# Kernel optimization log

Hardware: AMD Instinct MI355X
Metric: run time of the kernel (lower is better)

Reference implementation:

```python
import jax, jax.numpy as jnp
import numpy as np

B, D, N, MSRC, H = 4, 256, 2048, 2048, 4
DIM = D // H  # per-head dim = 64
EPS = 1e-3


def _conv1x1(W, b, z):
    # 1x1 Conv1d == per-position linear: W [out,in], z [B,in,N]
    return jnp.einsum('oc,bcn->bon', W, z) + b[None, :, None]


def setup_inputs() -> dict:
    key = jax.random.key(0)
    ks = jax.random.split(key, 20)
    s = 0.05
    x = jax.random.normal(ks[0], (B, D, N), dtype=jnp.float32)
    source = jax.random.normal(ks[1], (B, D, MSRC), dtype=jnp.float32)
    mask = (jax.random.uniform(ks[2], (B, N, MSRC)) > 0.3).astype(jnp.float32)
    Wq = jax.random.normal(ks[3], (D, D), jnp.float32) * s
    bq = jax.random.normal(ks[4], (D,), jnp.float32) * s
    Wk = jax.random.normal(ks[5], (D, D), jnp.float32) * s
    bk = jax.random.normal(ks[6], (D,), jnp.float32) * s
    Wv = jax.random.normal(ks[7], (D, D), jnp.float32) * s
    bv = jax.random.normal(ks[8], (D,), jnp.float32) * s
    Wm = jax.random.normal(ks[9], (D, D), jnp.float32) * s
    bm = jax.random.normal(ks[10], (D,), jnp.float32) * s
    W1 = jax.random.normal(ks[11], (2 * D, 2 * D), jnp.float32) * s
    b1 = jax.random.normal(ks[12], (2 * D,), jnp.float32) * s
    gamma = jnp.ones((2 * D,), jnp.float32)
    beta = jnp.zeros((2 * D,), jnp.float32)
    rmean = jax.random.normal(ks[13], (2 * D,), jnp.float32) * 0.1
    rvar = jax.random.uniform(ks[14], (2 * D,), jnp.float32) + 0.5
    W2 = jax.random.normal(ks[15], (D, 2 * D), jnp.float32) * s
    b2 = jnp.zeros((D,), jnp.float32)  # nn.init.constant_(mlp[-1].bias, 0.0)
    return dict(x=x, source=source, mask=mask, Wq=Wq, bq=bq, Wk=Wk, bk=bk,
                Wv=Wv, bv=bv, Wm=Wm, bm=bm, W1=W1, b1=b1, gamma=gamma,
                beta=beta, rmean=rmean, rvar=rvar, W2=W2, b2=b2)


def reference(x, source, mask, Wq, bq, Wk, bk, Wv, bv, Wm, bm,
              W1, b1, gamma, beta, rmean, rvar, W2, b2):
    b = x.shape[0]
    # channel dim split as (dim, heads) per torch .view(B, dim, H, -1)
    q = _conv1x1(Wq, bq, x).reshape(b, DIM, H, -1)        # [B,d,H,N]
    k = _conv1x1(Wk, bk, source).reshape(b, DIM, H, -1)   # [B,d,H,M]
    v = _conv1x1(Wv, bv, source).reshape(b, DIM, H, -1)   # [B,d,H,M]
    scores = jnp.einsum('bdhn,bdhm->bhnm', q, k) / (DIM ** 0.5)
    neg = -jnp.finfo(scores.dtype).max
    scores = jnp.where(mask[:, None, :, :] > 0, scores, neg)
    prob = jax.nn.softmax(scores, axis=-1)                # [B,H,N,M]
    msg = jnp.einsum('bhnm,bdhm->bdhn', prob, v).reshape(b, D, -1)
    message = _conv1x1(Wm, bm, msg)                       # [B,D,N]
    y = jnp.concatenate([x, message], axis=1)             # [B,2D,N]
    h = _conv1x1(W1, b1, y)
    # BatchNorm1d (eval mode, eps=1e-3)
    h = (h - rmean[None, :, None]) * jax.lax.rsqrt(rvar + EPS)[None, :, None]
    h = h * gamma[None, :, None] + beta[None, :, None]
    h = jax.nn.relu(h)
    return _conv1x1(W2, b2, h)                            # [B,D,N]
```

## Files before the change

### kernel.cpp

```cpp
#include <hip/hip_runtime.h>

constexpr int Bb = 4;
constexpr int Dd = 256;
constexpr int Nn = 2048;
constexpr int Mm = 2048;
constexpr int Hh = 4;
constexpr int D2 = 512;
constexpr int NT = Bb * Nn;

#define FMAXV 3.402823466e38f

typedef _Float16 half8 __attribute__((ext_vector_type(8)));
typedef _Float16 half4v __attribute__((ext_vector_type(4)));
typedef float f32x4 __attribute__((ext_vector_type(4)));

typedef const __attribute__((address_space(1))) void* gas_p;
typedef __attribute__((address_space(3))) void* las_p;

__device__ __forceinline__ void gload16(const void* g, void* l) {
    __builtin_amdgcn_global_load_lds((gas_p)g, (las_p)l, 16, 0, 0);
}

__global__ __launch_bounds__(256)
void prep_weights_kernel(const float* __restrict__ Wq, const float* __restrict__ bq,
                         const float* __restrict__ Wk, const float* __restrict__ bk,
                         const float* __restrict__ Wv, const float* __restrict__ bv,
                         const float* __restrict__ Wm,
                         const float* __restrict__ W1, const float* __restrict__ b1,
                         const float* __restrict__ gamma, const float* __restrict__ beta,
                         const float* __restrict__ rmean, const float* __restrict__ rvar,
                         const float* __restrict__ W2, const float* __restrict__ mask,
                         _Float16* __restrict__ Wqp, float* __restrict__ bqp,
                         _Float16* __restrict__ Wkvp, float* __restrict__ bkvp,
                         _Float16* __restrict__ Wmp,
                         _Float16* __restrict__ W1p, float* __restrict__ b1f,
                         _Float16* __restrict__ W2p,
                         unsigned long long* __restrict__ bmask) {
    const int r = blockIdx.x, t = threadIdx.x;
    if (r < 256) {
        const int h = r >> 6, d = r & 63, so = d * Hh + h;
        Wqp[r * 256 + t] = (_Float16)Wq[so * 256 + t];
        if (t == 0) bqp[r] = bq[so];
    } else if (r < 768) {
        const int rr = r - 256, part = rr >> 8, o = rr & 255;
        const int h = o >> 6, d = o & 63, so = d * Hh + h;
        const float* Ws = part ? Wv : Wk;
        const float* bs = part ? bv : bk;
        Wkvp[rr * 256 + t] = (_Float16)Ws[so * 256 + t];
        if (t == 0) bkvp[rr] = bs[so];
    } else if (r < 1024) {
        const int o = r - 768;
        const int h = t >> 6, d = t & 63, sk = d * Hh + h;
        Wmp[o * 256 + t] = (_Float16)Wm[o * 256 + sk];
    } else if (r < 1536) {
        const int o = r - 1024;
        const float s = gamma[o] * rsqrtf(rvar[o] + 1e-3f);
        W1p[o * 512 + t]       = (_Float16)(W1[o * 512 + t] * s);
        W1p[o * 512 + t + 256] = (_Float16)(W1[o * 512 + t + 256] * s);
        if (t == 0) b1f[o] = (b1[o] - rmean[o]) * s + beta[o];
    } else if (r < 1792) {
        const int o = r - 1536;
        W2p[o * 512 + t]       = (_Float16)W2[o * 512 + t];
        W2p[o * 512 + t + 256] = (_Float16)W2[o * 512 + t + 256];
    } else {
        const int id = r - 1792;
        const int w = t >> 6, lane = t & 63;
        const int row = id * 4 + w;
        const float* mrow = mask + (size_t)row * Mm;
        unsigned long long* brow = bmask + (size_t)row * (Mm / 64);
        #pragma unroll 4
        for (int word = 0; word < Mm / 64; ++word) {
            const float v = mrow[word * 64 + lane];
            const unsigned long long bits = __ballot(v > 0.f);
            if (lane == 0) brow[word] = bits;
        }
    }
}

__global__ __launch_bounds__(256)
void prep_x_kernel(const float* __restrict__ x, const float* __restrict__ source,
                   _Float16* __restrict__ Yp, _Float16* __restrict__ Sp) {
    __shared__ _Float16 Ts[64][72];
    const int z = blockIdx.z, b = z >> 1, which = z & 1;
    const float* src = which ? source : x;
    _Float16* dst = which ? Sp : Yp;
    const int stride = which ? 256 : 512;
    const int c0 = blockIdx.y * 64, n0 = blockIdx.x * 64;
    const int t = threadIdx.x;
    const int cl = t >> 2, np = (t & 3) * 16;
    const float* sp = src + ((size_t)b * Dd + c0 + cl) * Nn + n0 + np;
    #pragma unroll
    for (int i = 0; i < 4; ++i) {
        float4 v = *(const float4*)(sp + i * 4);
        Ts[np + i * 4 + 0][cl] = (_Float16)v.x;
        Ts[np + i * 4 + 1][cl] = (_Float16)v.y;
        Ts[np + i * 4 + 2][cl] = (_Float16)v.z;
        Ts[np + i * 4 + 3][cl] = (_Float16)v.w;
    }
    __syncthreads();
    const int nl = t >> 2, cp = (t & 3) * 16;
    half8 a0 = *(const half8*)&Ts[nl][cp];
    half8 a1 = *(const half8*)&Ts[nl][cp + 8];
    _Float16* dp = dst + ((size_t)b * Nn + n0 + nl) * stride + c0 + cp;
    *(half8*)dp = a0;
    *(half8*)(dp + 8) = a1;
}

__global__ __launch_bounds__(256)
void gemm4w_kernel(const _Float16* __restrict__ A, const _Float16* __restrict__ A2,
                   const _Float16* __restrict__ W, const float* __restrict__ bias,
                   _Float16* __restrict__ dst0, _Float16* __restrict__ dst1,
                   _Float16* __restrict__ dst2, float* __restrict__ dstF,
                   int K, int sA, int sOut, int modeSel, int relu) {
    __shared__ __align__(16) _Float16 As[2][128][64];
    __shared__ __align__(16) _Float16 Bs[2][128][64];
    __shared__ __align__(16) _Float16 Es[4][16][72];

    const int t = threadIdx.x;
    const int w = t >> 6, lane = t & 63, quad = lane >> 4, l16 = lane & 15;
    const int wr = w >> 1, wc = w & 1;
    const int n0 = blockIdx.x * 128;
    const int og0 = blockIdx.y * 128;

    int mode = 0, oloc0 = og0;
    const _Float16* Ab = A;
    int sAl = sA;
    _Float16* d0 = dst0;
    if (modeSel == 3) {
        const int part = blockIdx.y >> 1;
        if (part == 1)      { Ab = A2; sAl = 256; d0 = dst1; oloc0 = og0 - 256; }
        else if (part == 2) { Ab = A2; sAl = 256; mode = 1; oloc0 = og0 - 512; }
    } else if (modeSel == 2) {
        mode = 2;
    }

    const int srow = t >> 3, sslot = t & 7;
    const int schunk = sslot ^ (srow & 7);

    f32x4 acc[4][4] = {};

    const int nk = K / 64;
    int buf = 0;

    {
        #pragma unroll
        for (int c = 0; c < 4; ++c) {
            const int row = c * 32 + srow;
            gload16(Ab + (size_t)(n0 + row) * sAl + schunk * 8,
                    (_Float16*)As + c * 2048 + t * 8);
            gload16(W + (size_t)(og0 + row) * K + schunk * 8,
                    (_Float16*)Bs + c * 2048 + t * 8);
        }
        __asm__ volatile("s_waitcnt vmcnt(0)" ::: "memory");
        __syncthreads();
    }

    #pragma unroll 1
    for (int kt = 0; kt < nk; ++kt) {
        if (kt + 1 < nk) {
            const int k0 = (kt + 1) * 64, nb = buf ^ 1;
            #pragma unroll
            for (int c = 0; c < 4; ++c) {
                const int row = c * 32 + srow;
                gload16(Ab + (size_t)(n0 + row) * sAl + k0 + schunk * 8,
                        (_Float16*)As + nb * 8192 + c * 2048 + t * 8);
                gload16(W + (size_t)(og0 + row) * K + k0 + schunk * 8,
                        (_Float16*)Bs + nb * 8192 + c * 2048 + t * 8);
            }
        }
        #pragma unroll
        for (int ks = 0; ks < 2; ++ks) {
            const int csw = ((ks * 4 + quad) ^ (l16 & 7)) * 8;
            half8 af[4], bf[4];
            #pragma unroll
            for (int i = 0; i < 4; ++i)
                af[i] = *(const half8*)&As[buf][wr * 64 + i * 16 + l16][csw];
            #pragma unroll
            for (int j = 0; j < 4; ++j)
                bf[j] = *(const half8*)&Bs[buf][wc * 64 + j * 16 + l16][csw];
            #pragma unroll
            for (int i = 0; i < 4; ++i)
                #pragma unroll
                for (int j = 0; j < 4; ++j)
                    acc[i][j] = __builtin_amdgcn_mfma_f32_16x16x32_f16(af[i], bf[j], acc[i][j], 0, 0, 0);
        }
        if (kt + 1 < nk) {
            __asm__ volatile("s_waitcnt vmcnt(0)" ::: "memory");
            __syncthreads();
            buf ^= 1;
        }
    }

    float bcol[4];
    #pragma unroll
    for (int j = 0; j < 4; ++j) bcol[j] = bias[og0 + wc * 64 + j * 16 + l16];

    if (mode == 0) {
        #pragma unroll
        for (int i = 0; i < 4; ++i) {
            #pragma unroll
            for (int j = 0; j < 4; ++j)
                #pragma unroll
                for (int reg = 0; reg < 4; ++reg) {
                    float v = acc[i][j][reg] + bcol[j];
                    if (relu) v = fmaxf(v, 0.f);
                    Es[w][quad * 4 + reg][j * 16 + l16] = (_Float16)v;
                }
            __asm__ volatile("s_waitcnt lgkmcnt(0)" ::: "memory");
            const int row = lane & 15, oseg = (lane >> 4) * 16;
            half8 e0 = *(const half8*)&Es[w][row][oseg];
            half8 e1 = *(const half8*)&Es[w][row][oseg + 8];
            _Float16* dp = d0 + (size_t)(n0 + wr * 64 + i * 16 + row) * sOut
                         + oloc0 + wc * 64 + oseg;
            *(half8*)dp = e0;
            *(half8*)(dp + 8) = e1;
            __asm__ volatile("s_waitcnt lgkmcnt(0)" ::: "memory");
        }
    } else if (mode == 1) {
        #pragma unroll
        for (int i = 0; i < 4; ++i) {
            const int ng = n0 + wr * 64 + i * 16 + quad * 4;
            const int bidx = ng >> 11, m0 = ng & 2047;
            #pragma unroll
            for (int j = 0; j < 4; ++j) {
                const int o = oloc0 + wc * 64 + j * 16 + l16;
                half4v pv;
                #pragma unroll
                for (int reg = 0; reg < 4; ++reg) pv[reg] = (_Float16)(acc[i][j][reg] + bcol[j]);
                *(half4v*)(dst2 + ((size_t)bidx * 256 + o) * (size_t)Mm + m0) = pv;
            }
        }
    } else {
        #pragma unroll
        for (int i = 0; i < 4; ++i) {
            const int ng = n0 + wr * 64 + i * 16 + quad * 4;
            const int bidx = ng >> 11, m0 = ng & 2047;
            #pragma unroll
            for (int j = 0; j < 4; ++j) {
                const int o = og0 + wc * 64 + j * 16 + l16;
                f32x4 v;
                #pragma unroll
                for (int reg = 0; reg < 4; ++reg) v[reg] = acc[i][j][reg] + bcol[j];
                *(f32x4*)(dstF + ((size_t)bidx * 256 + o) * (size_t)Nn + m0) = v;
            }
        }
    }
}

__global__ __launch_bounds__(256)
void attn_mfma_kernel(const _Float16* __restrict__ Qp, const _Float16* __restrict__ Kp,
                      const _Float16* __restrict__ Vt,
                      const unsigned int* __restrict__ bmask,
                      _Float16* __restrict__ msgp) {
    __shared__ __align__(16) _Float16 Ks[2][64][72];
    __shared__ __align__(16) _Float16 Vs[2][64][72];
    __shared__ __align__(16) _Float16 Ps[4][16][72];

    const int b = blockIdx.z, h = blockIdx.y, n0 = blockIdx.x * 64;
    const int t = threadIdx.x;
    const int w = t >> 6, lane = t & 63, quad = lane >> 4, l16 = lane & 15;

    const _Float16* qp = Qp + ((size_t)b * Nn + n0 + w * 16 + l16) * 256 + h * 64 + quad * 8;
    const half8 qa0 = *(const half8*)(qp);
    const half8 qa1 = *(const half8*)(qp + 32);

    const _Float16* Kstg = Kp + (size_t)b * Nn * 256 + h * 64;
    const _Float16* Vstg = Vt + ((size_t)b * 256 + h * 64) * (size_t)Mm;
    const int sr = t >> 2, sc = (t & 3) * 16;

    const unsigned int* bmBase = bmask + ((size_t)b * Nn + n0 + w * 16 + quad * 4) * (Mm / 32);

    float lo[4] = {0.f, 0.f, 0.f, 0.f};
    f32x4 O[4] = {};

    half8 sk0, sk1, sv0, sv1;
    auto stage_load = [&](int m0) {
        const _Float16* ks = Kstg + (size_t)(m0 + sr) * 256 + sc;
        sk0 = *(const half8*)(ks);
        sk1 = *(const half8*)(ks + 8);
        const _Float16* vs = Vstg + (size_t)sr * Mm + m0 + sc;
        sv0 = *(const half8*)(vs);
        sv1 = *(const half8*)(vs + 8);
    };
    auto stage_write = [&](int buf) {
        *(half8*)&Ks[buf][sr][sc]     = sk0;
        *(half8*)&Ks[buf][sr][sc + 8] = sk1;
        *(half8*)&Vs[buf][sr][sc]     = sv0;
        *(half8*)&Vs[buf][sr][sc + 8] = sv1;
    };

    stage_load(0);
    stage_write(0);
    __syncthreads();

    #pragma unroll 1
    for (int it = 0; it < Mm / 64; ++it) {
        const int m0 = it * 64, cur = it & 1;
        if (it < Mm / 64 - 1) stage_load(m0 + 64);

        uint2 bmv[4];
        #pragma unroll
        for (int reg = 0; reg < 4; ++reg)
            bmv[reg] = *(const uint2*)(bmBase + (size_t)reg * (Mm / 32) + (m0 >> 5));

        f32x4 S[4];
        #pragma unroll
        for (int mt = 0; mt < 4; ++mt) {
            half8 k0 = *(const half8*)&Ks[cur][mt * 16 + l16][quad * 8];
            half8 k1 = *(const half8*)&Ks[cur][mt * 16 + l16][32 + quad * 8];
            f32x4 z = {0.f, 0.f, 0.f, 0.f};
            z = __builtin_amdgcn_mfma_f32_16x16x32_f16(qa0, k0, z, 0, 0, 0);
            z = __builtin_amdgcn_mfma_f32_16x16x32_f16(qa1, k1, z, 0, 0, 0);
            S[mt] = z;
        }

        float p[4][4];
        #pragma unroll
        for (int reg = 0; reg < 4; ++reg) {
            const unsigned losh = bmv[reg].x >> l16;
            const unsigned hish = bmv[reg].y >> l16;
            p[0][reg] = (losh & 1u)         ? __expf(S[0][reg] * 0.125f) : 0.f;
            p[1][reg] = ((losh >> 16) & 1u) ? __expf(S[1][reg] * 0.125f) : 0.f;
            p[2][reg] = (hish & 1u)         ? __expf(S[2][reg] * 0.125f) : 0.f;
            p[3][reg] = ((hish >> 16) & 1u) ? __expf(S[3][reg] * 0.125f) : 0.f;
        }
        #pragma unroll
        for (int reg = 0; reg < 4; ++reg)
            lo[reg] += (p[0][reg] + p[1][reg]) + (p[2][reg] + p[3][reg]);

        #pragma unroll
        for (int mt = 0; mt < 4; ++mt)
            #pragma unroll
            for (int reg = 0; reg < 4; ++reg)
                Ps[w][quad * 4 + reg][mt * 16 + l16] = (_Float16)p[mt][reg];
        __asm__ volatile("s_waitcnt lgkmcnt(0)" ::: "memory");
        half8 pa0 = *(const half8*)&Ps[w][l16][quad * 8];
        half8 pa1 = *(const half8*)&Ps[w][l16][32 + quad * 8];

        #pragma unroll
        for (int dt = 0; dt < 4; ++dt) {
            half8 v0 = *(const half8*)&Vs[cur][dt * 16 + l16][quad * 8];
            half8 v1 = *(const half8*)&Vs[cur][dt * 16 + l16][32 + quad * 8];
            O[dt] = __builtin_amdgcn_mfma_f32_16x16x32_f16(pa0, v0, O[dt], 0, 0, 0);
            O[dt] = __builtin_amdgcn_mfma_f32_16x16x32_f16(pa1, v1, O[dt], 0, 0, 0);
        }

        if (it < Mm / 64 - 1) stage_write(cur ^ 1);
        __syncthreads();
    }

    #pragma unroll
    for (int reg = 0; reg < 4; ++reg) {
        float s = lo[reg];
        s += __shfl_xor(s, 1);
        s += __shfl_xor(s, 2);
        s += __shfl_xor(s, 4);
        s += __shfl_xor(s, 8);
        lo[reg] = 1.0f / s;
    }

    _Float16* op = msgp + ((size_t)b * Nn + n0 + w * 16 + quad * 4) * 256 + h * 64 + l16;
    #pragma unroll
    for (int reg = 0; reg < 4; ++reg)
        #pragma unroll
        for (int dt = 0; dt < 4; ++dt)
            op[(size_t)reg * 256 + dt * 16] = (_Float16)(O[dt][reg] * lo[reg]);
}

extern "C" void kernel_launch(void* const* d_in, const int* in_sizes, int n_in,
                              void* d_out, int out_size, void* d_ws, size_t ws_size,
                              hipStream_t stream) {
    const float* x      = (const float*)d_in[0];
    const float* source = (const float*)d_in[1];
    const float* mask   = (const float*)d_in[2];
    const float* Wq = (const float*)d_in[3];
    const float* bq = (const float*)d_in[4];
    const float* Wk = (const float*)d_in[5];
    const float* bk = (const float*)d_in[6];
    const float* Wv = (const float*)d_in[7];
    const float* bv = (const float*)d_in[8];
    const float* Wm = (const float*)d_in[9];
    const float* bm = (const float*)d_in[10];
    const float* W1 = (const float*)d_in[11];
    const float* b1 = (const float*)d_in[12];
    const float* gamma = (const float*)d_in[13];
    const float* beta  = (const float*)d_in[14];
    const float* rmean = (const float*)d_in[15];
    const float* rvar  = (const float*)d_in[16];
    const float* W2 = (const float*)d_in[17];
    const float* b2 = (const float*)d_in[18];
    float* outp = (float*)d_out;

    char* wsb = (char*)d_ws;
    _Float16* Yp   = (_Float16*)wsb;
    _Float16* Sp   = (_Float16*)(wsb + (8u << 20));
    _Float16* Qp   = (_Float16*)(wsb + (12u << 20));
    _Float16* Kp   = (_Float16*)(wsb + (16u << 20));
    _Float16* Vt   = (_Float16*)(wsb + (20u << 20));
    _Float16* msgp = (_Float16*)(wsb + (24u << 20));
    _Float16* Hp   = (_Float16*)(wsb + (28u << 20));
    unsigned long long* bmask = (unsigned long long*)(wsb + (28u << 20));
    char* wp = wsb + (36u << 20);
    _Float16* Wqp  = (_Float16*)wp;            wp += 256 * 256 * 2;
    _Float16* Wkvp = (_Float16*)wp;            wp += 512 * 256 * 2;
    _Float16* Wmp  = (_Float16*)wp;            wp += 256 * 256 * 2;
    _Float16* W1p  = (_Float16*)wp;            wp += 512 * 512 * 2;
    _Float16* W2p  = (_Float16*)wp;            wp += 256 * 512 * 2;
    float* bqp  = (float*)wp;                  wp += 256 * 4;
    float* bkvp = (float*)wp;                  wp += 512 * 4;
    float* b1f  = (float*)wp;                  wp += 512 * 4;

    prep_weights_kernel<<<3840, 256, 0, stream>>>(
        Wq, bq, Wk, bk, Wv, bv, Wm, W1, b1, gamma, beta, rmean, rvar, W2, mask,
        Wqp, bqp, Wkvp, bkvp, Wmp, W1p, b1f, W2p, bmask);

    dim3 gPrep(Nn / 64, Dd / 64, Bb * 2);
    prep_x_kernel<<<gPrep, 256, 0, stream>>>(x, source, Yp, Sp);

    gemm4w_kernel<<<dim3(NT / 128, 6), 256, 0, stream>>>(
        Yp, Sp, Wqp, bqp, Qp, Kp, Vt, nullptr, 256, 512, 256, 3, 0);

    dim3 gAttn(Nn / 64, Hh, Bb);
    attn_mfma_kernel<<<gAttn, 256, 0, stream>>>(Qp, Kp, Vt,
                                                (const unsigned int*)bmask, msgp);

    gemm4w_kernel<<<dim3(NT / 128, 2), 256, 0, stream>>>(
        msgp, nullptr, Wmp, bm, Yp + 256, nullptr, nullptr, nullptr, 256, 256, 512, 0, 0);
    gemm4w_kernel<<<dim3(NT / 128, 4), 256, 0, stream>>>(
        Yp, nullptr, W1p, b1f, Hp, nullptr, nullptr, nullptr, 512, 512, 512, 0, 1);
    gemm4w_kernel<<<dim3(NT / 128, 2), 256, 0, stream>>>(
        Hp, nullptr, W2p, b2, nullptr, nullptr, nullptr, outp, 512, 512, 0, 2, 0);
}
```

Baseline: 248.8 us.

## Split attention over key halves, shrink GEMM tiles, fuse prep kernels

Attention is split into two halves along the key dimension with an XCD-aware block mapping. Each half writes unnormalized partial outputs and row sums, and a new combine kernel merges them. This is meant to double the attention grid for better occupancy. The 1/sqrt(d) scale is folded into the Q projection epilogue, and the attention tile drops double-buffered LDS in favour of extra syncs. GEMM output tiles shrink from 128x128 to 128x64 to double the block count, and the x/source transpose prep is merged into the weight prep kernel to save a launch. Risks are the extra combine pass, extra partial-result traffic, and the extra barriers in attention.

```diff
diff --git a/kernel.cpp b/kernel.cpp
--- a/kernel.cpp
+++ b/kernel.cpp
@@ -22,20 +22,22 @@
 }
 
 __global__ __launch_bounds__(256)
-void prep_weights_kernel(const float* __restrict__ Wq, const float* __restrict__ bq,
-                         const float* __restrict__ Wk, const float* __restrict__ bk,
-                         const float* __restrict__ Wv, const float* __restrict__ bv,
-                         const float* __restrict__ Wm,
-                         const float* __restrict__ W1, const float* __restrict__ b1,
-                         const float* __restrict__ gamma, const float* __restrict__ beta,
-                         const float* __restrict__ rmean, const float* __restrict__ rvar,
-                         const float* __restrict__ W2, const float* __restrict__ mask,
-                         _Float16* __restrict__ Wqp, float* __restrict__ bqp,
-                         _Float16* __restrict__ Wkvp, float* __restrict__ bkvp,
-                         _Float16* __restrict__ Wmp,
-                         _Float16* __restrict__ W1p, float* __restrict__ b1f,
-                         _Float16* __restrict__ W2p,
-                         unsigned long long* __restrict__ bmask) {
+void prep_all_kernel(const float* __restrict__ Wq, const float* __restrict__ bq,
+                     const float* __restrict__ Wk, const float* __restrict__ bk,
+                     const float* __restrict__ Wv, const float* __restrict__ bv,
+                     const float* __restrict__ Wm,
+                     const float* __restrict__ W1, const float* __restrict__ b1,
+                     const float* __restrict__ gamma, const float* __restrict__ beta,
+                     const float* __restrict__ rmean, const float* __restrict__ rvar,
+                     const float* __restrict__ W2, const float* __restrict__ mask,
+                     const float* __restrict__ x, const float* __restrict__ source,
+                     _Float16* __restrict__ Wqp, float* __restrict__ bqp,
+                     _Float16* __restrict__ Wkvp, float* __restrict__ bkvp,
+                     _Float16* __restrict__ Wmp,
+                     _Float16* __restrict__ W1p, float* __restrict__ b1f,
+                     _Float16* __restrict__ W2p,
+                     unsigned long long* __restrict__ bmask,
+                     _Float16* __restrict__ Yp, _Float16* __restrict__ Sp) {
     const int r = blockIdx.x, t = threadIdx.x;
     if (r < 256) {
         const int h = r >> 6, d = r & 63, so = d * Hh + h;
@@ -62,7 +64,7 @@
         const int o = r - 1536;
         W2p[o * 512 + t]       = (_Float16)W2[o * 512 + t];
         W2p[o * 512 + t + 256] = (_Float16)W2[o * 512 + t + 256];
-    } else {
+    } else if (r < 3840) {
         const int id = r - 1792;
         const int w = t >> 6, lane = t & 63;
         const int row = id * 4 + w;
@@ -74,36 +76,32 @@
             const unsigned long long bits = __ballot(v > 0.f);
             if (lane == 0) brow[word] = bits;
         }
-    }
-}
-
-__global__ __launch_bounds__(256)
-void prep_x_kernel(const float* __restrict__ x, const float* __restrict__ source,
-                   _Float16* __restrict__ Yp, _Float16* __restrict__ Sp) {
-    __shared__ _Float16 Ts[64][72];
-    const int z = blockIdx.z, b = z >> 1, which = z & 1;
-    const float* src = which ? source : x;
-    _Float16* dst = which ? Sp : Yp;
-    const int stride = which ? 256 : 512;
-    const int c0 = blockIdx.y * 64, n0 = blockIdx.x * 64;
-    const int t = threadIdx.x;
-    const int cl = t >> 2, np = (t & 3) * 16;
-    const float* sp = src + ((size_t)b * Dd + c0 + cl) * Nn + n0 + np;
-    #pragma unroll
-    for (int i = 0; i < 4; ++i) {
-        float4 v = *(const float4*)(sp + i * 4);
-        Ts[np + i * 4 + 0][cl] = (_Float16)v.x;
-        Ts[np + i * 4 + 1][cl] = (_Float16)v.y;
-        Ts[np + i * 4 + 2][cl] = (_Float16)v.z;
-        Ts[np + i * 4 + 3][cl] = (_Float16)v.w;
-    }
-    __syncthreads();
-    const int nl = t >> 2, cp = (t & 3) * 16;
-    half8 a0 = *(const half8*)&Ts[nl][cp];
-    half8 a1 = *(const half8*)&Ts[nl][cp + 8];
-    _Float16* dp = dst + ((size_t)b * Nn + n0 + nl) * stride + c0 + cp;
-    *(half8*)dp = a0;
-    *(half8*)(dp + 8) = a1;
+    } else {
+        __shared__ _Float16 Ts[64][72];
+        const int px = r - 3840;
+        const int n0 = (px & 31) * 64, c0 = ((px >> 5) & 3) * 64;
+        const int z = px >> 7, b = z >> 1, which = z & 1;
+        const float* src = which ? source : x;
+        _Float16* dst = which ? Sp : Yp;
+        const int stride = which ? 256 : 512;
+        const int cl = t >> 2, np = (t & 3) * 16;
+        const float* sp = src + ((size_t)b * Dd + c0 + cl) * Nn + n0 + np;
+        #pragma unroll
+        for (int i = 0; i < 4; ++i) {
+            float4 v = *(const float4*)(sp + i * 4);
+            Ts[np + i * 4 + 0][cl] = (_Float16)v.x;
+            Ts[np + i * 4 + 1][cl] = (_Float16)v.y;
+            Ts[np + i * 4 + 2][cl] = (_Float16)v.z;
+            Ts[np + i * 4 + 3][cl] = (_Float16)v.w;
+        }
+        __syncthreads();
+        const int nl = t >> 2, cp = (t & 3) * 16;
+        half8 a0 = *(const half8*)&Ts[nl][cp];
+        half8 a1 = *(const half8*)&Ts[nl][cp + 8];
+        _Float16* dp = dst + ((size_t)b * Nn + n0 + nl) * stride + c0 + cp;
+        *(half8*)dp = a0;
+        *(half8*)(dp + 8) = a1;
+    }
 }
 
 __global__ __launch_bounds__(256)
@@ -111,25 +109,25 @@
                    const _Float16* __restrict__ W, const float* __restrict__ bias,
                    _Float16* __restrict__ dst0, _Float16* __restrict__ dst1,
                    _Float16* __restrict__ dst2, float* __restrict__ dstF,
-                   int K, int sA, int sOut, int modeSel, int relu) {
-    __shared__ __align__(16) _Float16 As[2][128][64];
-    __shared__ __align__(16) _Float16 Bs[2][128][64];
+                   int K, int sA, int sOut, int modeSel, int relu, float oscale) {
+    __shared__ __align__(16) _Float16 As[2 * 128 * 64];
+    __shared__ __align__(16) _Float16 Bs[2 * 64 * 64];
     __shared__ __align__(16) _Float16 Es[4][16][72];
 
     const int t = threadIdx.x;
     const int w = t >> 6, lane = t & 63, quad = lane >> 4, l16 = lane & 15;
-    const int wr = w >> 1, wc = w & 1;
     const int n0 = blockIdx.x * 128;
-    const int og0 = blockIdx.y * 128;
+    const int og0 = blockIdx.y * 64;
 
     int mode = 0, oloc0 = og0;
     const _Float16* Ab = A;
     int sAl = sA;
     _Float16* d0 = dst0;
+    float osc = oscale;
     if (modeSel == 3) {
-        const int part = blockIdx.y >> 1;
-        if (part == 1)      { Ab = A2; sAl = 256; d0 = dst1; oloc0 = og0 - 256; }
-        else if (part == 2) { Ab = A2; sAl = 256; mode = 1; oloc0 = og0 - 512; }
+        const int part = blockIdx.y >> 2;
+        if (part == 1)      { Ab = A2; sAl = 256; d0 = dst1; oloc0 = og0 - 256; osc = 1.0f; }
+        else if (part == 2) { Ab = A2; sAl = 256; mode = 1; oloc0 = og0 - 512; osc = 1.0f; }
     } else if (modeSel == 2) {
         mode = 2;
     }
@@ -137,20 +135,19 @@
     const int srow = t >> 3, sslot = t & 7;
     const int schunk = sslot ^ (srow & 7);
 
-    f32x4 acc[4][4] = {};
-
+    f32x4 acc[2][4] = {};
     const int nk = K / 64;
     int buf = 0;
 
     {
         #pragma unroll
-        for (int c = 0; c < 4; ++c) {
-            const int row = c * 32 + srow;
-            gload16(Ab + (size_t)(n0 + row) * sAl + schunk * 8,
-                    (_Float16*)As + c * 2048 + t * 8);
-            gload16(W + (size_t)(og0 + row) * K + schunk * 8,
-                    (_Float16*)Bs + c * 2048 + t * 8);
-        }
+        for (int c = 0; c < 4; ++c)
+            gload16(Ab + (size_t)(n0 + c * 32 + srow) * sAl + schunk * 8,
+                    As + c * 2048 + t * 8);
+        #pragma unroll
+        for (int c = 0; c < 2; ++c)
+            gload16(W + (size_t)(og0 + c * 32 + srow) * K + schunk * 8,
+                    Bs + c * 2048 + t * 8);
         __asm__ volatile("s_waitcnt vmcnt(0)" ::: "memory");
         __syncthreads();
     }
@@ -160,26 +157,26 @@
         if (kt + 1 < nk) {
             const int k0 = (kt + 1) * 64, nb = buf ^ 1;
             #pragma unroll
-            for (int c = 0; c < 4; ++c) {
-                const int row = c * 32 + srow;
-                gload16(Ab + (size_t)(n0 + row) * sAl + k0 + schunk * 8,
-                        (_Float16*)As + nb * 8192 + c * 2048 + t * 8);
-                gload16(W + (size_t)(og0 + row) * K + k0 + schunk * 8,
-                        (_Float16*)Bs + nb * 8192 + c * 2048 + t * 8);
-            }
+            for (int c = 0; c < 4; ++c)
+                gload16(Ab + (size_t)(n0 + c * 32 + srow) * sAl + k0 + schunk * 8,
+                        As + nb * 8192 + c * 2048 + t * 8);
+            #pragma unroll
+            for (int c = 0; c < 2; ++c)
+                gload16(W + (size_t)(og0 + c * 32 + srow) * K + k0 + schunk * 8,
+                        Bs + nb * 4096 + c * 2048 + t * 8);
         }
         #pragma unroll
         for (int ks = 0; ks < 2; ++ks) {
             const int csw = ((ks * 4 + quad) ^ (l16 & 7)) * 8;
-            half8 af[4], bf[4];
-            #pragma unroll
-            for (int i = 0; i < 4; ++i)
-                af[i] = *(const half8*)&As[buf][wr * 64 + i * 16 + l16][csw];
+            half8 af[2], bf[4];
+            #pragma unroll
+            for (int i = 0; i < 2; ++i)
+                af[i] = *(const half8*)&As[buf * 8192 + (w * 32 + i * 16 + l16) * 64 + csw];
             #pragma unroll
             for (int j = 0; j < 4; ++j)
-                bf[j] = *(const half8*)&Bs[buf][wc * 64 + j * 16 + l16][csw];
-            #pragma unroll
-            for (int i = 0; i < 4; ++i)
+                bf[j] = *(const half8*)&Bs[buf * 4096 + (j * 16 + l16) * 64 + csw];
+            #pragma unroll
+            for (int i = 0; i < 2; ++i)
                 #pragma unroll
                 for (int j = 0; j < 4; ++j)
                     acc[i][j] = __builtin_amdgcn_mfma_f32_16x16x32_f16(af[i], bf[j], acc[i][j], 0, 0, 0);
@@ -193,16 +190,16 @@
 
     float bcol[4];
     #pragma unroll
-    for (int j = 0; j < 4; ++j) bcol[j] = bias[og0 + wc * 64 + j * 16 + l16];
+    for (int j = 0; j < 4; ++j) bcol[j] = bias[og0 + j * 16 + l16];
 
     if (mode == 0) {
         #pragma unroll
-        for (int i = 0; i < 4; ++i) {
+        for (int i = 0; i < 2; ++i) {
             #pragma unroll
             for (int j = 0; j < 4; ++j)
                 #pragma unroll
                 for (int reg = 0; reg < 4; ++reg) {
-                    float v = acc[i][j][reg] + bcol[j];
+                    float v = (acc[i][j][reg] + bcol[j]) * osc;
                     if (relu) v = fmaxf(v, 0.f);
                     Es[w][quad * 4 + reg][j * 16 + l16] = (_Float16)v;
                 }
@@ -210,20 +207,19 @@
             const int row = lane & 15, oseg = (lane >> 4) * 16;
             half8 e0 = *(const half8*)&Es[w][row][oseg];
             half8 e1 = *(const half8*)&Es[w][row][oseg + 8];
-            _Float16* dp = d0 + (size_t)(n0 + wr * 64 + i * 16 + row) * sOut
-                         + oloc0 + wc * 64 + oseg;
+            _Float16* dp = d0 + (size_t)(n0 + w * 32 + i * 16 + row) * sOut + oloc0 + oseg;
             *(half8*)dp = e0;
             *(half8*)(dp + 8) = e1;
             __asm__ volatile("s_waitcnt lgkmcnt(0)" ::: "memory");
         }
     } else if (mode == 1) {
         #pragma unroll
-        for (int i = 0; i < 4; ++i) {
-            const int ng = n0 + wr * 64 + i * 16 + quad * 4;
+        for (int i = 0; i < 2; ++i) {
+            const int ng = n0 + w * 32 + i * 16 + quad * 4;
             const int bidx = ng >> 11, m0 = ng & 2047;
             #pragma unroll
             for (int j = 0; j < 4; ++j) {
-                const int o = oloc0 + wc * 64 + j * 16 + l16;
+                const int o = oloc0 + j * 16 + l16;
                 half4v pv;
                 #pragma unroll
                 for (int reg = 0; reg < 4; ++reg) pv[reg] = (_Float16)(acc[i][j][reg] + bcol[j]);
@@ -232,12 +228,12 @@
         }
     } else {
         #pragma unroll
-        for (int i = 0; i < 4; ++i) {
-            const int ng = n0 + wr * 64 + i * 16 + quad * 4;
+        for (int i = 0; i < 2; ++i) {
+            const int ng = n0 + w * 32 + i * 16 + quad * 4;
             const int bidx = ng >> 11, m0 = ng & 2047;
             #pragma unroll
             for (int j = 0; j < 4; ++j) {
-                const int o = og0 + wc * 64 + j * 16 + l16;
+                const int o = og0 + j * 16 + l16;
                 f32x4 v;
                 #pragma unroll
                 for (int reg = 0; reg < 4; ++reg) v[reg] = acc[i][j][reg] + bcol[j];
@@ -251,12 +247,20 @@
 void attn_mfma_kernel(const _Float16* __restrict__ Qp, const _Float16* __restrict__ Kp,
                       const _Float16* __restrict__ Vt,
                       const unsigned int* __restrict__ bmask,
-                      _Float16* __restrict__ msgp) {
-    __shared__ __align__(16) _Float16 Ks[2][64][72];
-    __shared__ __align__(16) _Float16 Vs[2][64][72];
+                      _Float16* __restrict__ Oa, _Float16* __restrict__ Ob,
+                      float* __restrict__ La, float* __restrict__ Lb) {
+    __shared__ __align__(16) _Float16 Ks[64][72];
+    __shared__ __align__(16) _Float16 Vs[64][72];
     __shared__ __align__(16) _Float16 Ps[4][16][72];
 
-    const int b = blockIdx.z, h = blockIdx.y, n0 = blockIdx.x * 64;
+    const int id = blockIdx.x;
+    const int xcd = id & 7, loc = id >> 3;
+    const int bh = xcd * 2 + (loc >> 6);
+    const int sub = loc & 63;
+    const int mhalf = sub & 1;
+    const int n0 = (sub >> 1) * 64;
+    const int b = bh >> 2, h = bh & 3;
+
     const int t = threadIdx.x;
     const int w = t >> 6, lane = t & 63, quad = lane >> 4, l16 = lane & 15;
 
@@ -269,6 +273,10 @@
     const int sr = t >> 2, sc = (t & 3) * 16;
 
     const unsigned int* bmBase = bmask + ((size_t)b * Nn + n0 + w * 16 + quad * 4) * (Mm / 32);
+
+    _Float16* Od = mhalf ? Ob : Oa;
+    float* Ld = mhalf ? Lb : La;
+    const int mbeg = mhalf * (Mm / 2);
 
     float lo[4] = {0.f, 0.f, 0.f, 0.f};
     f32x4 O[4] = {};
@@ -282,21 +290,21 @@
         sv0 = *(const half8*)(vs);
         sv1 = *(const half8*)(vs + 8);
     };
-    auto stage_write = [&](int buf) {
-        *(half8*)&Ks[buf][sr][sc]     = sk0;
-        *(half8*)&Ks[buf][sr][sc + 8] = sk1;
-        *(half8*)&Vs[buf][sr][sc]     = sv0;
-        *(half8*)&Vs[buf][sr][sc + 8] = sv1;
+    auto stage_write = [&]() {
+        *(half8*)&Ks[sr][sc]     = sk0;
+        *(half8*)&Ks[sr][sc + 8] = sk1;
+        *(half8*)&Vs[sr][sc]     = sv0;
+        *(half8*)&Vs[sr][sc + 8] = sv1;
     };
 
-    stage_load(0);
-    stage_write(0);
+    stage_load(mbeg);
+    stage_write();
     __syncthreads();
 
     #pragma unroll 1
-    for (int it = 0; it < Mm / 64; ++it) {
-        const int m0 = it * 64, cur = it & 1;
-        if (it < Mm / 64 - 1) stage_load(m0 + 64);
+    for (int it = 0; it < (Mm / 2) / 64; ++it) {
+        const int m0 = mbeg + it * 64;
+        if (it < (Mm / 2) / 64 - 1) stage_load(m0 + 64);
 
         uint2 bmv[4];
         #pragma unroll
@@ -306,8 +314,8 @@
         f32x4 S[4];
         #pragma unroll
         for (int mt = 0; mt < 4; ++mt) {
-            half8 k0 = *(const half8*)&Ks[cur][mt * 16 + l16][quad * 8];
-            half8 k1 = *(const half8*)&Ks[cur][mt * 16 + l16][32 + quad * 8];
+            half8 k0 = *(const half8*)&Ks[mt * 16 + l16][quad * 8];
+            half8 k1 = *(const half8*)&Ks[mt * 16 + l16][32 + quad * 8];
             f32x4 z = {0.f, 0.f, 0.f, 0.f};
             z = __builtin_amdgcn_mfma_f32_16x16x32_f16(qa0, k0, z, 0, 0, 0);
             z = __builtin_amdgcn_mfma_f32_16x16x32_f16(qa1, k1, z, 0, 0, 0);
@@ -319,10 +327,10 @@
         for (int reg = 0; reg < 4; ++reg) {
             const unsigned losh = bmv[reg].x >> l16;
             const unsigned hish = bmv[reg].y >> l16;
-            p[0][reg] = (losh & 1u)         ? __expf(S[0][reg] * 0.125f) : 0.f;
-            p[1][reg] = ((losh >> 16) & 1u) ? __expf(S[1][reg] * 0.125f) : 0.f;
-            p[2][reg] = (hish & 1u)         ? __expf(S[2][reg] * 0.125f) : 0.f;
-            p[3][reg] = ((hish >> 16) & 1u) ? __expf(S[3][reg] * 0.125f) : 0.f;
+            p[0][reg] = (losh & 1u)         ? __expf(S[0][reg]) : 0.f;
+            p[1][reg] = ((losh >> 16) & 1u) ? __expf(S[1][reg]) : 0.f;
+            p[2][reg] = (hish & 1u)         ? __expf(S[2][reg]) : 0.f;
+            p[3][reg] = ((hish >> 16) & 1u) ? __expf(S[3][reg]) : 0.f;
         }
         #pragma unroll
         for (int reg = 0; reg < 4; ++reg)
@@ -339,14 +347,17 @@
 
         #pragma unroll
         for (int dt = 0; dt < 4; ++dt) {
-            half8 v0 = *(const half8*)&Vs[cur][dt * 16 + l16][quad * 8];
-            half8 v1 = *(const half8*)&Vs[cur][dt * 16 + l16][32 + quad * 8];
+            half8 v0 = *(const half8*)&Vs[dt * 16 + l16][quad * 8];
+            half8 v1 = *(const half8*)&Vs[dt * 16 + l16][32 + quad * 8];
             O[dt] = __builtin_amdgcn_mfma_f32_16x16x32_f16(pa0, v0, O[dt], 0, 0, 0);
             O[dt] = __builtin_amdgcn_mfma_f32_16x16x32_f16(pa1, v1, O[dt], 0, 0, 0);
         }
 
-        if (it < Mm / 64 - 1) stage_write(cur ^ 1);
-        __syncthreads();
+        if (it < (Mm / 2) / 64 - 1) {
+            __syncthreads();
+            stage_write();
+            __syncthreads();
+        }
     }
 
     #pragma unroll
@@ -356,15 +367,38 @@
         s += __shfl_xor(s, 2);
         s += __shfl_xor(s, 4);
         s += __shfl_xor(s, 8);
-        lo[reg] = 1.0f / s;
-    }
-
-    _Float16* op = msgp + ((size_t)b * Nn + n0 + w * 16 + quad * 4) * 256 + h * 64 + l16;
+        lo[reg] = s;
+    }
+
+    _Float16* op = Od + ((size_t)b * Nn + n0 + w * 16 + quad * 4) * 256 + h * 64 + l16;
     #pragma unroll
     for (int reg = 0; reg < 4; ++reg)
         #pragma unroll
         for (int dt = 0; dt < 4; ++dt)
-            op[(size_t)reg * 256 + dt * 16] = (_Float16)(O[dt][reg] * lo[reg]);
+            op[(size_t)reg * 256 + dt * 16] = (_Float16)(O[dt][reg] * 0.0625f);
+    if (l16 == 0) {
+        #pragma unroll
+        for (int reg = 0; reg < 4; ++reg)
+            Ld[((size_t)b * Nn + n0 + w * 16 + quad * 4 + reg) * 4 + h] = lo[reg] * 0.0625f;
+    }
+}
+
+__global__ __launch_bounds__(256)
+void combine_kernel(const _Float16* __restrict__ Oa, const _Float16* __restrict__ Ob,
+                    const float* __restrict__ La, const float* __restrict__ Lb,
+                    _Float16* __restrict__ out) {
+    const int gid = blockIdx.x * 256 + threadIdx.x;
+    const int row = gid >> 5, chunk = gid & 31;
+    const int h = chunk >> 3;
+    const float L = La[row * 4 + h] + Lb[row * 4 + h];
+    const float inv = 1.0f / L;
+    half8 a = *(const half8*)(Oa + (size_t)row * 256 + chunk * 8);
+    half8 c = *(const half8*)(Ob + (size_t)row * 256 + chunk * 8);
+    half8 o;
+    #pragma unroll
+    for (int k = 0; k < 8; ++k)
+        o[k] = (_Float16)(((float)a[k] + (float)c[k]) * inv);
+    *(half8*)(out + (size_t)row * 256 + chunk * 8) = o;
 }
 
 extern "C" void kernel_launch(void* const* d_in, const int* in_sizes, int n_in,
@@ -400,6 +434,9 @@
     _Float16* msgp = (_Float16*)(wsb + (24u << 20));
     _Float16* Hp   = (_Float16*)(wsb + (28u << 20));
     unsigned long long* bmask = (unsigned long long*)(wsb + (28u << 20));
+    _Float16* Ob = (_Float16*)(wsb + (30u << 20));
+    float* La = (float*)(wsb + (34u << 20));
+    float* Lb = (float*)(wsb + (34u << 20) + (128u << 10));
     char* wp = wsb + (36u << 20);
     _Float16* Wqp  = (_Float16*)wp;            wp += 256 * 256 * 2;
     _Float16* Wkvp = (_Float16*)wp;            wp += 512 * 256 * 2;
@@ -410,24 +447,23 @@
     float* bkvp = (float*)wp;                  wp += 512 * 4;
     float* b1f  = (float*)wp;                  wp += 512 * 4;
 
-    prep_weights_kernel<<<3840, 256, 0, stream>>>(
+    prep_all_kernel<<<4864, 256, 0, stream>>>(
         Wq, bq, Wk, bk, Wv, bv, Wm, W1, b1, gamma, beta, rmean, rvar, W2, mask,
-        Wqp, bqp, Wkvp, bkvp, Wmp, W1p, b1f, W2p, bmask);
-
-    dim3 gPrep(Nn / 64, Dd / 64, Bb * 2);
-    prep_x_kernel<<<gPrep, 256, 0, stream>>>(x, source, Yp, Sp);
-
-    gemm4w_kernel<<<dim3(NT / 128, 6), 256, 0, stream>>>(
-        Yp, Sp, Wqp, bqp, Qp, Kp, Vt, nullptr, 256, 512, 256, 3, 0);
-
-    dim3 gAttn(Nn / 64, Hh, Bb);
-    attn_mfma_kernel<<<gAttn, 256, 0, stream>>>(Qp, Kp, Vt,
-                                                (const unsigned int*)bmask, msgp);
-
-    gemm4w_kernel<<<dim3(NT / 128, 2), 256, 0, stream>>>(
-        msgp, nullptr, Wmp, bm, Yp + 256, nullptr, nullptr, nullptr, 256, 256, 512, 0, 0);
+        x, source, Wqp, bqp, Wkvp, bkvp, Wmp, W1p, b1f, W2p, bmask, Yp, Sp);
+
+    gemm4w_kernel<<<dim3(NT / 128, 12), 256, 0, stream>>>(
+        Yp, Sp, Wqp, bqp, Qp, Kp, Vt, nullptr, 256, 512, 256, 3, 0, 0.125f);
+
+    attn_mfma_kernel<<<1024, 256, 0, stream>>>(Qp, Kp, Vt,
+                                               (const unsigned int*)bmask,
+                                               msgp, Ob, La, Lb);
+
+    combine_kernel<<<1024, 256, 0, stream>>>(msgp, Ob, La, Lb, Sp);
+
     gemm4w_kernel<<<dim3(NT / 128, 4), 256, 0, stream>>>(
-        Yp, nullptr, W1p, b1f, Hp, nullptr, nullptr, nullptr, 512, 512, 512, 0, 1);
-    gemm4w_kernel<<<dim3(NT / 128, 2), 256, 0, stream>>>(
-        Hp, nullptr, W2p, b2, nullptr, nullptr, nullptr, outp, 512, 512, 0, 2, 0);
-}
+        Sp, nullptr, Wmp, bm, Yp + 256, nullptr, nullptr, nullptr, 256, 256, 512, 0, 0, 1.0f);
+    gemm4w_kernel<<<dim3(NT / 128, 8), 256, 0, stream>>>(
+        Yp, nullptr, W1p, b1f, Hp, nullptr, nullptr, nullptr, 512, 512, 512, 0, 1, 1.0f);
+    gemm4w_kernel<<<dim3(NT / 128, 4), 256, 0, stream>>>(
+        Hp, nullptr, W2p, b2, nullptr, nullptr, nullptr, outp, 512, 512, 0, 2, 0, 1.0f);
+}
```

Result: faster. 237.7 us (-4.5%).
